# Kernel optimization log

Measured on AMD Instinct MI355X. Metric: run time of the kernel, lower is better.

Reference implementation:

```python
import jax, jax.numpy as jnp
import numpy as np

N = 2_000_000
VOXEL_SIZE = (0.1, 0.1, 0.1)
PC_RANGE = (-50.0, -50.0, -5.0, 50.0, 50.0, 3.0)
NUM_BATCHES = 4


def setup_inputs() -> dict:
    key = jax.random.key(0)
    k1, k2 = jax.random.split(key)
    pmin = jnp.array(PC_RANGE[:3], dtype=jnp.float32)
    pmax = jnp.array(PC_RANGE[3:], dtype=jnp.float32)
    # points uniformly distributed over the configured point-cloud range
    points = jax.random.uniform(k1, (N, 3), dtype=jnp.float32, minval=pmin, maxval=pmax)
    batch_indices = jnp.sort(jax.random.randint(k2, (N,), 0, NUM_BATCHES, dtype=jnp.int32))
    return {"points": points, "batch_indices": batch_indices}


def reference(points, batch_indices):
    """Vectorized equivalent of PointVoxelizer.forward.

    Returns fixed-shape (jit-friendly) analogues of the torch outputs:
      voxel_coords   [N, 4] int32  [batch, z, y, x], padded rows = -1
      voxel_features [N, 3] float32 voxel centers, padded rows = 0
      point_to_voxel_map [N] int32, -1 for invalid points
      n_voxels       scalar int32, number of real (non-padding) voxels
    The per-batch torch.unique + offset concatenation is reproduced exactly by
    a single sorted unique over the combined hash batch*GRID + cell_hash,
    since unique sorts and the hash is lexicographic in (batch, x, y, z).
    """
    dtype = points.dtype
    vsize = jnp.array(VOXEL_SIZE, dtype=dtype)
    pmin = jnp.array(PC_RANGE[:3], dtype=dtype)
    pmax = jnp.array(PC_RANGE[3:], dtype=dtype)

    vc = jnp.floor((points - pmin) / vsize).astype(jnp.int32)  # [N,3] (x,y,z)
    grid = jnp.ceil((pmax - pmin) / vsize).astype(jnp.int32)   # [3] = (1000,1000,80)
    valid = jnp.all(vc >= 0, axis=1) & jnp.all(vc < grid, axis=1)  # [N]

    YZ = grid[1] * grid[2]
    GXYZ = grid[0] * YZ  # cells per batch element (8e7 < 2^31/NUM_BATCHES)
    cell_hash = vc[:, 0] * YZ + vc[:, 1] * grid[2] + vc[:, 2]
    SENTINEL = jnp.iinfo(jnp.int32).max
    combined = jnp.where(valid, batch_indices.astype(jnp.int32) * GXYZ + cell_hash, SENTINEL)

    uniq, inv = jnp.unique(combined, return_inverse=True, size=N, fill_value=SENTINEL)
    is_real = uniq != SENTINEL  # padding (and any invalid-point bucket) masked out

    point_to_voxel_map = jnp.where(valid, inv.reshape(-1).astype(jnp.int32), -1)

    b = uniq // GXYZ
    rem = uniq % GXYZ
    x = rem // YZ
    y = (rem % YZ) // grid[2]
    z = rem % grid[2]

    coords_bzyx = jnp.stack([b, z, y, x], axis=1).astype(jnp.int32)  # [N,4]
    voxel_coords = jnp.where(is_real[:, None], coords_bzyx, -1)

    xyz = jnp.stack([x, y, z], axis=1).astype(dtype)
    centers = pmin + (xyz + 0.5) * vsize
    voxel_features = jnp.where(is_real[:, None], centers, jnp.zeros((), dtype))

    n_voxels = is_real.sum().astype(jnp.int32)
    return voxel_coords, voxel_features, point_to_voxel_map, n_voxels
```

## Files before the change

kernel.cpp:

```cpp
#include <hip/hip_runtime.h>


namespace {

constexpr int GX = 1000, GY = 1000, GZ = 80;
constexpr int YZ = GY * GZ;
constexpr int GXYZ = GX * YZ;
constexpr int TOTAL_CELLS = GXYZ * 4;
constexpr int BBITS = 18;
constexpr int BCELLS = 1 << BBITS;
constexpr int NB = (TOTAL_CELLS + BCELLS - 1) >> BBITS;
constexpr int BWORDS = BCELLS / 32;
constexpr int NCHUNK = 512;
static_assert(NCHUNK % 64 == 0, "k2a wave scan");

constexpr size_t OFF_PK    = 8000000;
constexpr size_t OFF_POS   = 16000000;
constexpr size_t OFF_MVAL  = 24000000;
constexpr size_t OFF_DK    = 32000000;
constexpr size_t OFF_HIST  = 40000000;
constexpr size_t OFF_TOT   = 43000000;
constexpr size_t OFF_BOFF  = 43100000;
constexpr size_t OFF_DCNT  = 43200000;
constexpr size_t OFF_DRANK = 43300000;

__device__ __forceinline__ int sw(int w) {
  return ((w & 7) << 10) | (w >> 3);
}

__global__ void k1_keys_hist(const float* __restrict__ pts, const int* __restrict__ bi,
                             unsigned* __restrict__ upt, unsigned* __restrict__ hist,
                             int n, int cpb) {
  __shared__ unsigned h[NB];
  const int c = blockIdx.x;
  for (int b = threadIdx.x; b < NB; b += blockDim.x) h[b] = 0;
  __syncthreads();
  const int lo = c * cpb, hi = min(n, lo + cpb);
  for (int i = lo + threadIdx.x; i < hi; i += blockDim.x) {
    float px = pts[3 * i + 0], py = pts[3 * i + 1], pz = pts[3 * i + 2];
    int vx = (int)floorf((px + 50.0f) / 0.1f);
    int vy = (int)floorf((py + 50.0f) / 0.1f);
    int vz = (int)floorf((pz + 5.0f) / 0.1f);
    bool valid = (vx >= 0) & (vy >= 0) & (vz >= 0) & (vx < GX) & (vy < GY) & (vz < GZ);
    unsigned u = 0xFFFFFFFFu;
    if (valid) {
      u = (unsigned)(bi[i] * GXYZ + vx * YZ + vy * GZ + vz);
      atomicAdd(&h[u >> BBITS], 1u);
    }
    upt[i] = u;
  }
  __syncthreads();
  for (int b = threadIdx.x; b < NB; b += blockDim.x)
    hist[(size_t)c * NB + b] = h[b];
}

__global__ void k2a_chunk_pre(unsigned* __restrict__ hist, unsigned* __restrict__ tot) {
  const int wid = (blockIdx.x * blockDim.x + threadIdx.x) >> 6;
  const int lane = threadIdx.x & 63;
  if (wid >= NB) return;
  unsigned run = 0;
  for (int c0 = 0; c0 < NCHUNK; c0 += 64) {
    const size_t idx = (size_t)(c0 + lane) * NB + wid;
    unsigned v = hist[idx];
    unsigned inc = v;
    for (int o = 1; o < 64; o <<= 1) {
      unsigned t = __shfl_up(inc, o);
      if (lane >= o) inc += t;
    }
    hist[idx] = run + inc - v;
    run += __shfl(inc, 63);
  }
  if (lane == 63) tot[wid] = run;
}

__global__ void k2b_scan_tot(const unsigned* __restrict__ tot, unsigned* __restrict__ boff) {
  __shared__ unsigned s[1024];
  const int tid = threadIdx.x;
  unsigned v0 = (2 * tid     < NB) ? tot[2 * tid]     : 0u;
  unsigned v1 = (2 * tid + 1 < NB) ? tot[2 * tid + 1] : 0u;
  unsigned t = v0 + v1;
  s[tid] = t;
  __syncthreads();
  for (int o = 1; o < 1024; o <<= 1) {
    unsigned add = (tid >= o) ? s[tid - o] : 0u;
    __syncthreads();
    s[tid] += add;
    __syncthreads();
  }
  unsigned excl = s[tid] - t;
  if (2 * tid     < NB) boff[2 * tid]     = excl;
  if (2 * tid + 1 < NB) boff[2 * tid + 1] = excl + v0;
  if (tid == 1023) boff[NB] = s[1023];
}

__global__ void k3_scatter(const unsigned* __restrict__ upt, const unsigned* __restrict__ hist,
                           const unsigned* __restrict__ boff, unsigned* __restrict__ pk,
                           unsigned* __restrict__ pos, int n, int cpb) {
  __shared__ unsigned cur[NB];
  const int c = blockIdx.x;
  for (int b = threadIdx.x; b < NB; b += blockDim.x)
    cur[b] = boff[b] + hist[(size_t)c * NB + b];
  __syncthreads();
  const int lo = c * cpb, hi = min(n, lo + cpb);
  for (int i = lo + threadIdx.x; i < hi; i += blockDim.x) {
    unsigned u = upt[i];
    if (u == 0xFFFFFFFFu) continue;
    unsigned p = atomicAdd(&cur[u >> BBITS], 1u);
    pk[p] = u;
    pos[i] = p;
  }
}

__global__ void __launch_bounds__(1024) k4_rank(
    const unsigned* __restrict__ pk, const unsigned* __restrict__ boff,
    unsigned* __restrict__ dcnt, unsigned* __restrict__ dk,
    unsigned* __restrict__ mapval) {
  __shared__ unsigned bits[BWORDS];
  __shared__ unsigned wpre[BWORDS];
  __shared__ unsigned s[1024];
  const int tid = threadIdx.x;
  const int bid = blockIdx.x;

  for (int w = tid; w < BWORDS; w += 1024) bits[w] = 0;
  __syncthreads();
  const unsigned lo = boff[bid], hi = boff[bid + 1];
  const unsigned base = (unsigned)bid << BBITS;
  for (unsigned p = lo + tid; p < hi; p += 1024) {
    unsigned local = pk[p] - base;
    atomicOr(&bits[sw(local >> 5)], 1u << (local & 31));
  }
  __syncthreads();

  unsigned c8[8];
  unsigned t = 0;
  #pragma unroll
  for (int j = 0; j < 8; j++) {
    unsigned p = __popc(bits[j * 1024 + tid]);
    c8[j] = t;
    t += p;
  }
  s[tid] = t;
  __syncthreads();
  for (int o = 1; o < 1024; o <<= 1) {
    unsigned add = (tid >= o) ? s[tid - o] : 0u;
    __syncthreads();
    s[tid] += add;
    __syncthreads();
  }
  const unsigned excl = s[tid] - t;
  #pragma unroll
  for (int j = 0; j < 8; j++) wpre[j * 1024 + tid] = excl + c8[j];
  if (tid == 1023) dcnt[bid] = s[1023];
  __syncthreads();

  const unsigned dkb = lo;
  #pragma unroll
  for (int j = 0; j < 8; j++) {
    const int slot = j * 1024 + tid;
    unsigned m = bits[slot];
    unsigned r = wpre[slot];
    const unsigned lbase = (unsigned)(tid * 8 + j) << 5;
    while (m) {
      int bit = __ffs(m) - 1;
      m &= m - 1;
      dk[dkb + r] = base + lbase + (unsigned)bit;
      r++;
    }
  }

  for (unsigned p = lo + tid; p < hi; p += 1024) {
    unsigned local = pk[p] - base;
    int slot = sw((int)(local >> 5));
    mapval[p] = wpre[slot] + (unsigned)__popc(bits[slot] & ((1u << (local & 31)) - 1u));
  }
}

__global__ void k6_emit(const unsigned* __restrict__ dk, const unsigned* __restrict__ boff,
                        const unsigned* __restrict__ dcnt, unsigned* __restrict__ drank_tbl,
                        float* __restrict__ out_coords, float* __restrict__ out_feats,
                        float* __restrict__ out_nvox, int n) {
  __shared__ unsigned s[256];
  const int tid = threadIdx.x;
  const int bid = blockIdx.x;

  if (bid >= NB) {
    unsigned part = 0;
    for (int k = tid; k < NB; k += 256) part += dcnt[k];
    s[tid] = part;
    __syncthreads();
    for (int o = 128; o > 0; o >>= 1) {
      if (tid < o) s[tid] += s[tid + o];
      __syncthreads();
    }
    const unsigned nv = s[0];
    if (bid == NB && tid == 0) *out_nvox = (float)nv;
    const int row = (bid - NB) * 256 + tid;
    if (row < n && (unsigned)row >= nv) {
      float* c = out_coords + (size_t)row * 4;
      c[0] = -1.0f; c[1] = -1.0f; c[2] = -1.0f; c[3] = -1.0f;
      float* f = out_feats + (size_t)row * 3;
      f[0] = 0.0f; f[1] = 0.0f; f[2] = 0.0f;
    }
    return;
  }

  unsigned part = 0;
  for (int k = tid; k < bid; k += 256) part += dcnt[k];
  s[tid] = part;
  __syncthreads();
  for (int o = 128; o > 0; o >>= 1) {
    if (tid < o) s[tid] += s[tid + o];
    __syncthreads();
  }
  const unsigned drank = s[0];
  if (tid == 0) drank_tbl[bid] = drank;

  const unsigned dc = dcnt[bid];
  const unsigned dkb = boff[bid];
  for (unsigned j = tid; j < dc; j += 256) {
    unsigned u = dk[dkb + j];
    int bat = (int)(u / (unsigned)GXYZ);
    int rem = (int)(u % (unsigned)GXYZ);
    int x = rem / YZ, ry = rem % YZ;
    int y = ry / GZ, z = ry % GZ;
    const size_t r = drank + j;
    float* cc = out_coords + r * 4;
    cc[0] = (float)bat; cc[1] = (float)z; cc[2] = (float)y; cc[3] = (float)x;
    float* ff = out_feats + r * 3;
    ff[0] = -50.0f + ((float)x + 0.5f) * 0.1f;
    ff[1] = -50.0f + ((float)y + 0.5f) * 0.1f;
    ff[2] = -5.0f + ((float)z + 0.5f) * 0.1f;
  }
}

__global__ void k7_map(const unsigned* __restrict__ upt, const unsigned* __restrict__ pos,
                       const unsigned* __restrict__ mapval, const unsigned* __restrict__ drank_tbl,
                       float* __restrict__ out_map, int n) {
  int i = blockIdx.x * blockDim.x + threadIdx.x;
  if (i >= n) return;
  unsigned u = upt[i];
  if (u == 0xFFFFFFFFu) {
    out_map[i] = -1.0f;
    return;
  }
  out_map[i] = (float)(drank_tbl[u >> BBITS] + mapval[pos[i]]);
}

}

extern "C" void kernel_launch(void* const* d_in, const int* in_sizes, int n_in,
                              void* d_out, int out_size, void* d_ws, size_t ws_size,
                              hipStream_t stream) {
  const int N = in_sizes[0] / 3;
  const float* pts = (const float*)d_in[0];
  const int* bi = (const int*)d_in[1];
  float* out = (float*)d_out;

  unsigned* upt   = (unsigned*)d_ws;
  unsigned* pk    = (unsigned*)((char*)d_ws + OFF_PK);
  unsigned* pos   = (unsigned*)((char*)d_ws + OFF_POS);
  unsigned* mval  = (unsigned*)((char*)d_ws + OFF_MVAL);
  unsigned* dk    = (unsigned*)((char*)d_ws + OFF_DK);
  unsigned* hist  = (unsigned*)((char*)d_ws + OFF_HIST);
  unsigned* tot   = (unsigned*)((char*)d_ws + OFF_TOT);
  unsigned* boff  = (unsigned*)((char*)d_ws + OFF_BOFF);
  unsigned* dcnt  = (unsigned*)((char*)d_ws + OFF_DCNT);
  unsigned* drank = (unsigned*)((char*)d_ws + OFF_DRANK);

  float* out_coords = out;
  float* out_feats  = out + 4LL * N;
  float* out_map    = out + 7LL * N;
  float* out_nvox   = out + 8LL * N;

  const int cpb = (N + NCHUNK - 1) / NCHUNK;
  const int pad_blocks = (N + 255) / 256;

  k1_keys_hist<<<NCHUNK, 256, 0, stream>>>(pts, bi, upt, hist, N, cpb);
  k2a_chunk_pre<<<(NB * 64 + 255) / 256, 256, 0, stream>>>(hist, tot);
  k2b_scan_tot<<<1, 1024, 0, stream>>>(tot, boff);
  k3_scatter<<<NCHUNK, 256, 0, stream>>>(upt, hist, boff, pk, pos, N, cpb);
  k4_rank<<<NB, 1024, 0, stream>>>(pk, boff, dcnt, dk, mval);
  k6_emit<<<NB + pad_blocks, 256, 0, stream>>>(dk, boff, dcnt, drank,
                                               out_coords, out_feats, out_nvox, N);
  k7_map<<<(N + 255) / 256, 256, 0, stream>>>(upt, pos, mval, drank, out_map, N);
}
```

Measured before the change: 177.6 us.

## Use wave-shuffle block scans and precompute voxel rank offsets in a separate scan kernel

Replaces the shared-memory Hillis-Steele block scans (many __syncthreads) in k2b and k4_rank with wave-level shuffle scans plus a small per-wave offset array. It moves the per-block prefix sum of distinct counts out of k6_emit, where every block redundantly reduced dcnt, into a new single-block k5 scan kernel that also writes n_voxels. It also uses register-held prefixes in k4's emit loop. This adds one kernel launch in exchange for removing redundant reductions from the roughly 8000 padding blocks in k6.

```diff
diff --git a/kernel.cpp b/kernel.cpp
--- a/kernel.cpp
+++ b/kernel.cpp
@@ -13,6 +13,7 @@
 constexpr int BWORDS = BCELLS / 32;
 constexpr int NCHUNK = 512;
 static_assert(NCHUNK % 64 == 0, "k2a wave scan");
+static_assert(NB <= 2048, "1-block scans assume <=2048 elements");
 
 constexpr size_t OFF_PK    = 8000000;
 constexpr size_t OFF_POS   = 16000000;
@@ -73,24 +74,43 @@
   if (lane == 63) tot[wid] = run;
 }
 
-__global__ void k2b_scan_tot(const unsigned* __restrict__ tot, unsigned* __restrict__ boff) {
-  __shared__ unsigned s[1024];
+__device__ __forceinline__ void scan_block_2048(const unsigned* __restrict__ src,
+                                                unsigned* __restrict__ dst, int nb,
+                                                bool write_end, float* out_total) {
+  __shared__ unsigned s16[16];
   const int tid = threadIdx.x;
-  unsigned v0 = (2 * tid     < NB) ? tot[2 * tid]     : 0u;
-  unsigned v1 = (2 * tid + 1 < NB) ? tot[2 * tid + 1] : 0u;
+  const int lane = tid & 63, wid = tid >> 6;
+  unsigned v0 = (2 * tid     < nb) ? src[2 * tid]     : 0u;
+  unsigned v1 = (2 * tid + 1 < nb) ? src[2 * tid + 1] : 0u;
   unsigned t = v0 + v1;
-  s[tid] = t;
-  __syncthreads();
-  for (int o = 1; o < 1024; o <<= 1) {
-    unsigned add = (tid >= o) ? s[tid - o] : 0u;
-    __syncthreads();
-    s[tid] += add;
-    __syncthreads();
-  }
-  unsigned excl = s[tid] - t;
-  if (2 * tid     < NB) boff[2 * tid]     = excl;
-  if (2 * tid + 1 < NB) boff[2 * tid + 1] = excl + v0;
-  if (tid == 1023) boff[NB] = s[1023];
+  unsigned incl = t;
+  #pragma unroll
+  for (int o = 1; o < 64; o <<= 1) {
+    unsigned u = __shfl_up(incl, o);
+    if (lane >= o) incl += u;
+  }
+  if (lane == 63) s16[wid] = incl;
+  __syncthreads();
+  unsigned woff = 0;
+  for (int j = 0; j < wid; j++) woff += s16[j];
+  unsigned excl = woff + incl - t;
+  if (2 * tid     < nb) dst[2 * tid]     = excl;
+  if (2 * tid + 1 < nb) dst[2 * tid + 1] = excl + v0;
+  if (tid == 1023) {
+    if (write_end) dst[nb] = excl + t;
+    if (out_total) *out_total = (float)(excl + t);
+  }
+}
+
+__global__ void __launch_bounds__(1024) k2b_scan_tot(const unsigned* __restrict__ tot,
+                                                     unsigned* __restrict__ boff) {
+  scan_block_2048(tot, boff, NB, true, nullptr);
+}
+
+__global__ void __launch_bounds__(1024) k5_scan_dcnt(const unsigned* __restrict__ dcnt,
+                                                     unsigned* __restrict__ drank_tbl,
+                                                     float* __restrict__ out_nvox) {
+  scan_block_2048(dcnt, drank_tbl, NB, false, out_nvox);
 }
 
 __global__ void k3_scatter(const unsigned* __restrict__ upt, const unsigned* __restrict__ hist,
@@ -117,9 +137,10 @@
     unsigned* __restrict__ mapval) {
   __shared__ unsigned bits[BWORDS];
   __shared__ unsigned wpre[BWORDS];
-  __shared__ unsigned s[1024];
+  __shared__ unsigned s16[16];
   const int tid = threadIdx.x;
   const int bid = blockIdx.x;
+  const int lane = tid & 63, wid = tid >> 6;
 
   for (int w = tid; w < BWORDS; w += 1024) bits[w] = 0;
   __syncthreads();
@@ -139,26 +160,26 @@
     c8[j] = t;
     t += p;
   }
-  s[tid] = t;
-  __syncthreads();
-  for (int o = 1; o < 1024; o <<= 1) {
-    unsigned add = (tid >= o) ? s[tid - o] : 0u;
-    __syncthreads();
-    s[tid] += add;
-    __syncthreads();
-  }
-  const unsigned excl = s[tid] - t;
+  unsigned incl = t;
+  #pragma unroll
+  for (int o = 1; o < 64; o <<= 1) {
+    unsigned u = __shfl_up(incl, o);
+    if (lane >= o) incl += u;
+  }
+  if (lane == 63) s16[wid] = incl;
+  __syncthreads();
+  unsigned woff = 0;
+  for (int j = 0; j < wid; j++) woff += s16[j];
+  const unsigned excl = woff + incl - t;
   #pragma unroll
   for (int j = 0; j < 8; j++) wpre[j * 1024 + tid] = excl + c8[j];
-  if (tid == 1023) dcnt[bid] = s[1023];
-  __syncthreads();
+  if (tid == 1023) dcnt[bid] = excl + t;
 
   const unsigned dkb = lo;
   #pragma unroll
   for (int j = 0; j < 8; j++) {
-    const int slot = j * 1024 + tid;
-    unsigned m = bits[slot];
-    unsigned r = wpre[slot];
+    unsigned m = bits[j * 1024 + tid];
+    unsigned r = excl + c8[j];
     const unsigned lbase = (unsigned)(tid * 8 + j) << 5;
     while (m) {
       int bit = __ffs(m) - 1;
@@ -167,6 +188,7 @@
       r++;
     }
   }
+  __syncthreads();
 
   for (unsigned p = lo + tid; p < hi; p += 1024) {
     unsigned local = pk[p] - base;
@@ -176,24 +198,14 @@
 }
 
 __global__ void k6_emit(const unsigned* __restrict__ dk, const unsigned* __restrict__ boff,
-                        const unsigned* __restrict__ dcnt, unsigned* __restrict__ drank_tbl,
-                        float* __restrict__ out_coords, float* __restrict__ out_feats,
-                        float* __restrict__ out_nvox, int n) {
-  __shared__ unsigned s[256];
+                        const unsigned* __restrict__ dcnt, const unsigned* __restrict__ drank_tbl,
+                        const float* __restrict__ nvox_f,
+                        float* __restrict__ out_coords, float* __restrict__ out_feats, int n) {
   const int tid = threadIdx.x;
   const int bid = blockIdx.x;
 
   if (bid >= NB) {
-    unsigned part = 0;
-    for (int k = tid; k < NB; k += 256) part += dcnt[k];
-    s[tid] = part;
-    __syncthreads();
-    for (int o = 128; o > 0; o >>= 1) {
-      if (tid < o) s[tid] += s[tid + o];
-      __syncthreads();
-    }
-    const unsigned nv = s[0];
-    if (bid == NB && tid == 0) *out_nvox = (float)nv;
+    const unsigned nv = (unsigned)*nvox_f;
     const int row = (bid - NB) * 256 + tid;
     if (row < n && (unsigned)row >= nv) {
       float* c = out_coords + (size_t)row * 4;
@@ -204,17 +216,7 @@
     return;
   }
 
-  unsigned part = 0;
-  for (int k = tid; k < bid; k += 256) part += dcnt[k];
-  s[tid] = part;
-  __syncthreads();
-  for (int o = 128; o > 0; o >>= 1) {
-    if (tid < o) s[tid] += s[tid + o];
-    __syncthreads();
-  }
-  const unsigned drank = s[0];
-  if (tid == 0) drank_tbl[bid] = drank;
-
+  const unsigned drank = drank_tbl[bid];
   const unsigned dc = dcnt[bid];
   const unsigned dkb = boff[bid];
   for (unsigned j = tid; j < dc; j += 256) {
@@ -280,7 +282,8 @@
   k2b_scan_tot<<<1, 1024, 0, stream>>>(tot, boff);
   k3_scatter<<<NCHUNK, 256, 0, stream>>>(upt, hist, boff, pk, pos, N, cpb);
   k4_rank<<<NB, 1024, 0, stream>>>(pk, boff, dcnt, dk, mval);
-  k6_emit<<<NB + pad_blocks, 256, 0, stream>>>(dk, boff, dcnt, drank,
-                                               out_coords, out_feats, out_nvox, N);
+  k5_scan_dcnt<<<1, 1024, 0, stream>>>(dcnt, drank, out_nvox);
+  k6_emit<<<NB + pad_blocks, 256, 0, stream>>>(dk, boff, dcnt, drank, out_nvox,
+                                               out_coords, out_feats, N);
   k7_map<<<(N + 255) / 256, 256, 0, stream>>>(upt, pos, mval, drank, out_map, N);
 }
```

Measured after the change: 175.3 us. No clear change (-1.3%).
